# Optimization experiments

Measured on AMD Instinct MI355X. Metric: run time of the kernel, lower is better.

## Reference

```python
import jax, jax.numpy as jnp
import numpy as np

N_NEURONS, D_MODEL, D_FF, N_PATTERNS, K_PATTERNS = 2048, 1024, 4096, 64, 4
B, S, K = 4, 2048, 8


def setup_inputs() -> dict:
    key = jax.random.key(0)
    ks = jax.random.split(key, 10)
    return {
        "x": jax.random.normal(ks[0], (B, S, D_MODEL), jnp.float32),
        "router_out": jax.random.normal(ks[1], (B, S, D_MODEL), jnp.float32),
        "topk_neuron_idx": jax.random.randint(ks[2], (B, S, K), 0, N_NEURONS),
        "topk_neuron_weights": jax.random.uniform(ks[3], (B, S, K), jnp.float32),
        "selected_neurons": jax.random.normal(ks[4], (B, S, K, D_MODEL), jnp.float32),
        "pattern_queries": jax.random.normal(ks[5], (N_PATTERNS, D_MODEL), jnp.float32) * 0.02,
        "gates": jax.random.normal(ks[6], (N_PATTERNS, D_FF), jnp.float32) * 0.02,
        "up_w": jax.random.normal(ks[7], (D_FF, D_MODEL), jnp.float32) / np.sqrt(D_MODEL),
        "up_b": jnp.zeros((D_FF,), jnp.float32),
        "down_w": jax.random.normal(ks[8], (D_MODEL, D_FF), jnp.float32) / np.sqrt(D_FF),
        "down_b": jnp.zeros((D_MODEL,), jnp.float32),
    }


def reference(x, router_out, topk_neuron_idx, topk_neuron_weights, selected_neurons,
              pattern_queries, gates, up_w, up_b, down_w, down_b):
    D = selected_neurons.shape[-1]
    # pattern scoring: [P, B, S, K]
    sim = jnp.einsum('pd,bskd->pbsk', pattern_queries, selected_neurons) / jnp.sqrt(jnp.float32(D))
    pattern_scores = jnp.einsum('pbsk,bsk->bsp', sim, topk_neuron_weights)  # weighted sum over K, permuted
    topk_scores, topk_pattern_idx = jax.lax.top_k(pattern_scores, K_PATTERNS)  # [B,S,k]
    topk_pattern_weights = jax.nn.softmax(topk_scores, axis=-1)
    selected_gates = gates[topk_pattern_idx]  # [B,S,k,d_ff]
    ffn_gate = jnp.einsum('bsk,bskf->bsf', topk_pattern_weights, selected_gates)
    h = jnp.einsum('bsd,fd->bsf', x, up_w) + up_b
    h = jax.nn.gelu(h * jax.nn.sigmoid(ffn_gate), approximate=False)
    return jnp.einsum('bsf,df->bsd', h, down_w) + down_b
```

## Files before the change

### kernel.cpp

```cpp
#include <hip/hip_runtime.h>
#include <hip/hip_bf16.h>
#include <math.h>

#define R_   8192
#define DM   1024
#define DFF  4096
#define NP   64
#define KN   8

typedef __bf16 bf16x8 __attribute__((ext_vector_type(8)));
typedef float  f32x4  __attribute__((ext_vector_type(4)));

__device__ __forceinline__ unsigned short f2bf(float f) {
  union { float f; unsigned u; } v; v.f = f;
  unsigned u = v.u;
  return (unsigned short)((u + 0x7FFFu + ((u >> 16) & 1u)) >> 16);
}

__device__ __forceinline__ float dot4(const float4 a, const float4 b) {
  return a.x * b.x + a.y * b.y + a.z * b.z + a.w * b.w;
}

__device__ __forceinline__ void fma4(float4& a, float w, const float4 s) {
  a.x += w * s.x; a.y += w * s.y; a.z += w * s.z; a.w += w * s.w;
}

__global__ __launch_bounds__(256) void cvt_bf16_kernel(
    const float* __restrict__ in, unsigned short* __restrict__ out, int n8) {
  int i = blockIdx.x * 256 + threadIdx.x;
  if (i >= n8) return;
  const float4* p = (const float4*)in + (size_t)i * 2;
  float4 a = p[0], b = p[1];
  uint4 r;
  r.x = (unsigned)f2bf(a.x) | ((unsigned)f2bf(a.y) << 16);
  r.y = (unsigned)f2bf(a.z) | ((unsigned)f2bf(a.w) << 16);
  r.z = (unsigned)f2bf(b.x) | ((unsigned)f2bf(b.y) << 16);
  r.w = (unsigned)f2bf(b.z) | ((unsigned)f2bf(b.w) << 16);
  ((uint4*)out)[i] = r;
}

__global__ __launch_bounds__(256) void vcomp_kernel(
    const float* __restrict__ sn,
    const float* __restrict__ tw,
    float* __restrict__ v)
{
  const int r = blockIdx.x;
  const int t = threadIdx.x;
  float w[KN];
#pragma unroll
  for (int k = 0; k < KN; ++k) w[k] = tw[(size_t)r * KN + k];
  const float* base = sn + (size_t)r * (KN * DM) + t * 4;
  float4 a = {0.f, 0.f, 0.f, 0.f};
#pragma unroll
  for (int k = 0; k < KN; ++k) fma4(a, w[k], *(const float4*)(base + k * DM));
  *(float4*)(v + (size_t)r * DM + t * 4) = a;
}

__global__ __launch_bounds__(256, 2) void score_kernel(
    const float* __restrict__ v,
    const float* __restrict__ pq,
    int*   __restrict__ out_idx,
    float* __restrict__ out_w)
{
  const int lane = threadIdx.x & 63;
  const int wave = threadIdx.x >> 6;
  const int pos0 = (blockIdx.x * 4 + wave) * 4;

  float4 vr[4][4];
#pragma unroll
  for (int p = 0; p < 4; ++p) {
    const float4* s = (const float4*)(v + (size_t)(pos0 + p) * DM + lane * 16);
    vr[p][0] = s[0]; vr[p][1] = s[1]; vr[p][2] = s[2]; vr[p][3] = s[3];
  }

  float sreg[4];
#pragma unroll 1
  for (int pat = 0; pat < NP; ++pat) {
    const float4* q = (const float4*)(pq + pat * DM + lane * 16);
    const float4 q0 = q[0], q1 = q[1], q2 = q[2], q3 = q[3];
    float part[4];
#pragma unroll
    for (int p = 0; p < 4; ++p)
      part[p] = dot4(q0, vr[p][0]) + dot4(q1, vr[p][1]) +
                dot4(q2, vr[p][2]) + dot4(q3, vr[p][3]);
#pragma unroll
    for (int off = 32; off >= 1; off >>= 1) {
#pragma unroll
      for (int p = 0; p < 4; ++p)
        part[p] += __shfl_xor(part[p], off, 64);
    }
    if (lane == pat) {
#pragma unroll
      for (int p = 0; p < 4; ++p) sreg[p] = part[p] * 0.03125f;
    }
  }

#pragma unroll
  for (int p = 0; p < 4; ++p) {
    float cur = sreg[p];
    float m0, m1, m2, m3; int i0, i1, i2, i3;
#define ARGMAX_STEP(MV, MI)                                   \
    {                                                         \
      float bv = cur; int bi = lane;                          \
      _Pragma("unroll")                                       \
      for (int off = 32; off >= 1; off >>= 1) {               \
        float ov = __shfl_xor(bv, off, 64);                   \
        int   oi = __shfl_xor(bi, off, 64);                   \
        if (ov > bv || (ov == bv && oi < bi)) { bv = ov; bi = oi; } \
      }                                                       \
      MV = bv; MI = bi;                                       \
      if (lane == bi) cur = -3.0e38f;                         \
    }
    ARGMAX_STEP(m0, i0) ARGMAX_STEP(m1, i1) ARGMAX_STEP(m2, i2) ARGMAX_STEP(m3, i3)
#undef ARGMAX_STEP
    const float e1 = __expf(m1 - m0), e2 = __expf(m2 - m0), e3 = __expf(m3 - m0);
    const float inv = 1.f / (1.f + e1 + e2 + e3);
    if (lane < 4) {
      const int r = pos0 + p;
      const int myi = (lane == 0) ? i0 : (lane == 1) ? i1 : (lane == 2) ? i2 : i3;
      const float mye = (lane == 0) ? 1.f : (lane == 1) ? e1 : (lane == 2) ? e2 : e3;
      out_idx[r * 4 + lane] = myi;
      out_w[r * 4 + lane] = mye * inv;
    }
  }
}

__device__ __forceinline__ void gll16(const void* g, void* l) {
  __builtin_amdgcn_global_load_lds(
      (const __attribute__((address_space(1))) unsigned int*)g,
      (__attribute__((address_space(3))) unsigned int*)l, 16, 0, 0);
}

template <int K, int N, int MODE>
__global__ __launch_bounds__(256, 2) void gemm_kernel(
    const unsigned short* __restrict__ A,
    const unsigned short* __restrict__ Bm,
    const float* __restrict__ bias,
    const int*   __restrict__ pidx,
    const float* __restrict__ pwt,
    const float* __restrict__ gates,
    void* __restrict__ Cout)
{
  __shared__ __align__(16) unsigned short As[128 * 32];
  __shared__ __align__(16) unsigned short Bs[128 * 32];
  const int tid  = threadIdx.x;
  const int lane = tid & 63;
  const int wid  = tid >> 6;
  const int wr   = wid >> 1;
  const int wc   = wid & 1;
  constexpr int NB = N / 128;
  const int brow = blockIdx.x / NB;
  const int bcol = blockIdx.x % NB;

  const unsigned short* Ab = A  + (size_t)brow * 128 * K;
  const unsigned short* Bb = Bm + (size_t)bcol * 128 * K;

  f32x4 acc[4][4];
#pragma unroll
  for (int m = 0; m < 4; ++m)
#pragma unroll
    for (int n = 0; n < 4; ++n)
      acc[m][n] = (f32x4){0.f, 0.f, 0.f, 0.f};

  const int srow = tid >> 2;
  const int scol = (tid & 3) * 8;
  char* ldsA = (char*)As + (tid >> 6) * 1024;
  char* ldsB = (char*)Bs + (tid >> 6) * 1024;

  const int arow = wr * 64 + (lane & 15);
  const int bro  = wc * 64 + (lane & 15);
  const int koff = (lane >> 4) * 8;

  for (int k0 = 0; k0 < K; k0 += 32) {
    if (k0) __syncthreads();
    gll16(Ab + (size_t)srow * K + k0 + scol,        ldsA);
    gll16(Ab + (size_t)(srow + 64) * K + k0 + scol, ldsA + 4096);
    gll16(Bb + (size_t)srow * K + k0 + scol,        ldsB);
    gll16(Bb + (size_t)(srow + 64) * K + k0 + scol, ldsB + 4096);
    __syncthreads();

    bf16x8 af[4], bfr[4];
#pragma unroll
    for (int m = 0; m < 4; ++m)
      af[m] = *(const bf16x8*)(As + (arow + m * 16) * 32 + koff);
#pragma unroll
    for (int n = 0; n < 4; ++n)
      bfr[n] = *(const bf16x8*)(Bs + (bro + n * 16) * 32 + koff);
#pragma unroll
    for (int m = 0; m < 4; ++m)
#pragma unroll
      for (int n = 0; n < 4; ++n)
        acc[m][n] = __builtin_amdgcn_mfma_f32_16x16x32_bf16(
            af[m], bfr[n], acc[m][n], 0, 0, 0);
  }

  const int crow0 = brow * 128 + wr * 64;
  const int ccol0 = bcol * 128 + wc * 64 + (lane & 15);
  const int rsub  = (lane >> 4) * 4;

  if (MODE == 0) {
    unsigned short* H = (unsigned short*)Cout;
#pragma unroll
    for (int m = 0; m < 4; ++m) {
      const int rbase = crow0 + m * 16 + rsub;
      int   ia[4][4];
      float wa[4][4];
#pragma unroll
      for (int j = 0; j < 4; ++j) {
        const int4   iq = *(const int4*)(pidx + (size_t)(rbase + j) * 4);
        const float4 wq = *(const float4*)(pwt + (size_t)(rbase + j) * 4);
        ia[j][0] = iq.x; ia[j][1] = iq.y; ia[j][2] = iq.z; ia[j][3] = iq.w;
        wa[j][0] = wq.x; wa[j][1] = wq.y; wa[j][2] = wq.z; wa[j][3] = wq.w;
      }
#pragma unroll
      for (int n = 0; n < 4; ++n) {
        const int col = ccol0 + n * 16;
        const float ub = bias[col];
#pragma unroll
        for (int j = 0; j < 4; ++j) {
          float g = wa[j][0] * gates[(size_t)ia[j][0] * DFF + col]
                  + wa[j][1] * gates[(size_t)ia[j][1] * DFF + col]
                  + wa[j][2] * gates[(size_t)ia[j][2] * DFF + col]
                  + wa[j][3] * gates[(size_t)ia[j][3] * DFF + col];
          const float u   = acc[m][n][j] + ub;
          const float val = u * (1.f / (1.f + __expf(-g)));
          const float h   = 0.5f * val * (1.f + erff(val * 0.70710678118654752f));
          H[(size_t)(rbase + j) * N + col] = f2bf(h);
        }
      }
    }
  } else {
    float* O = (float*)Cout;
#pragma unroll
    for (int m = 0; m < 4; ++m) {
      const int rbase = crow0 + m * 16 + rsub;
#pragma unroll
      for (int n = 0; n < 4; ++n) {
        const int col = ccol0 + n * 16;
        const float db = bias[col];
#pragma unroll
        for (int j = 0; j < 4; ++j)
          O[(size_t)(rbase + j) * N + col] = acc[m][n][j] + db;
      }
    }
  }
}

extern "C" void kernel_launch(void* const* d_in, const int* in_sizes, int n_in,
                              void* d_out, int out_size, void* d_ws, size_t ws_size,
                              hipStream_t stream) {
  const float* x     = (const float*)d_in[0];
  const float* tw    = (const float*)d_in[3];
  const float* sn    = (const float*)d_in[4];
  const float* pq    = (const float*)d_in[5];
  const float* gates = (const float*)d_in[6];
  const float* upw   = (const float*)d_in[7];
  const float* upb   = (const float*)d_in[8];
  const float* dnw   = (const float*)d_in[9];
  const float* dnb   = (const float*)d_in[10];
  float* out = (float*)d_out;

  char* p = (char*)d_ws;
  unsigned short* xb  = (unsigned short*)p; p += (size_t)R_ * DM * 2;
  unsigned short* uwb = (unsigned short*)p; p += (size_t)DFF * DM * 2;
  unsigned short* dwb = (unsigned short*)p; p += (size_t)DM * DFF * 2;
  unsigned short* H   = (unsigned short*)p; p += (size_t)R_ * DFF * 2;
  int*   pidx = (int*)p;   p += (size_t)R_ * 4 * sizeof(int);
  float* pwt  = (float*)p; p += (size_t)R_ * 4 * sizeof(float);
  float* vbuf = (float*)p; p += (size_t)R_ * DM * sizeof(float);

  cvt_bf16_kernel<<<(R_ * DM / 8) / 256, 256, 0, stream>>>(x, xb, R_ * DM / 8);
  cvt_bf16_kernel<<<(DFF * DM / 8) / 256, 256, 0, stream>>>(upw, uwb, DFF * DM / 8);
  cvt_bf16_kernel<<<(DM * DFF / 8) / 256, 256, 0, stream>>>(dnw, dwb, DM * DFF / 8);

  vcomp_kernel<<<R_, 256, 0, stream>>>(sn, tw, vbuf);
  score_kernel<<<R_ / 16, 256, 0, stream>>>(vbuf, pq, pidx, pwt);

  gemm_kernel<DM, DFF, 0><<<(R_ / 128) * (DFF / 128), 256, 0, stream>>>(
      xb, uwb, upb, pidx, pwt, gates, (void*)H);
  gemm_kernel<DFF, DM, 1><<<(R_ / 128) * (DM / 128), 256, 0, stream>>>(
      H, dwb, dnb, nullptr, nullptr, nullptr, (void*)out);
}
```

Measured before the change: 408.5 us.

## Rewrite GEMMs with larger tiles, multi-stage LDS ring and register double-buffering

```diff
diff --git a/kernel.cpp b/kernel.cpp
--- a/kernel.cpp
+++ b/kernel.cpp
@@ -131,8 +131,8 @@
       (__attribute__((address_space(3))) unsigned int*)l, 16, 0, 0);
 }
 
-template <int K, int N, int MODE>
-__global__ __launch_bounds__(256, 2) void gemm_kernel(
+template <int K, int N, int BM, int BN, int WM, int WN, int RING, int MODE>
+__global__ __launch_bounds__(512, 2) void gemm_kernel(
     const unsigned short* __restrict__ A,
     const unsigned short* __restrict__ Bm,
     const float* __restrict__ bias,
@@ -141,67 +141,122 @@
     const float* __restrict__ gates,
     void* __restrict__ Cout)
 {
-  __shared__ __align__(16) unsigned short As[128 * 32];
-  __shared__ __align__(16) unsigned short Bs[128 * 32];
+  extern __shared__ char smem[];
+  constexpr int NT     = K / 32;
+  constexpr int MF     = WM / 16;
+  constexpr int NF     = WN / 16;
+  constexpr int NWC    = BN / WN;
+  constexpr int LA     = BM / 128;
+  constexpr int LB     = BN / 128;
+  constexpr int KEEP   = (RING - 3) * (LA + LB);
+  constexpr int TILE_A = BM * 64;
+  constexpr int TILE   = TILE_A + BN * 64;
+  constexpr int NBN    = N / BN;
+
   const int tid  = threadIdx.x;
   const int lane = tid & 63;
   const int wid  = tid >> 6;
-  const int wr   = wid >> 1;
-  const int wc   = wid & 1;
-  constexpr int NB = N / 128;
-  const int brow = blockIdx.x / NB;
-  const int bcol = blockIdx.x % NB;
-
-  const unsigned short* Ab = A  + (size_t)brow * 128 * K;
-  const unsigned short* Bb = Bm + (size_t)bcol * 128 * K;
-
-  f32x4 acc[4][4];
-#pragma unroll
-  for (int m = 0; m < 4; ++m)
-#pragma unroll
-    for (int n = 0; n < 4; ++n)
+  const int wr   = wid / NWC;
+  const int wc   = wid % NWC;
+
+  const int grid = gridDim.x;
+  const int cpx  = grid >> 3;
+  const int swz  = (blockIdx.x & 7) * cpx + (blockIdx.x >> 3);
+  const int brow = swz / NBN;
+  const int bcol = swz % NBN;
+
+  const unsigned short* Ab = A  + (size_t)brow * BM * K;
+  const unsigned short* Bb = Bm + (size_t)bcol * BN * K;
+
+  int aoffE[LA], boffE[LB];
+#pragma unroll
+  for (int i = 0; i < LA; ++i)
+    aoffE[i] = (i * 128 + wid * 16 + (lane >> 2)) * K + (lane & 3) * 8;
+#pragma unroll
+  for (int i = 0; i < LB; ++i)
+    boffE[i] = (i * 128 + wid * 16 + (lane >> 2)) * K + (lane & 3) * 8;
+
+  const int ard = (wr * WM + (lane & 15)) * 64 + (lane >> 4) * 16;
+  const int brd = (wc * WN + (lane & 15)) * 64 + (lane >> 4) * 16;
+
+  f32x4 acc[MF][NF];
+#pragma unroll
+  for (int m = 0; m < MF; ++m)
+#pragma unroll
+    for (int n = 0; n < NF; ++n)
       acc[m][n] = (f32x4){0.f, 0.f, 0.f, 0.f};
 
-  const int srow = tid >> 2;
-  const int scol = (tid & 3) * 8;
-  char* ldsA = (char*)As + (tid >> 6) * 1024;
-  char* ldsB = (char*)Bs + (tid >> 6) * 1024;
-
-  const int arow = wr * 64 + (lane & 15);
-  const int bro  = wc * 64 + (lane & 15);
-  const int koff = (lane >> 4) * 8;
-
-  for (int k0 = 0; k0 < K; k0 += 32) {
-    if (k0) __syncthreads();
-    gll16(Ab + (size_t)srow * K + k0 + scol,        ldsA);
-    gll16(Ab + (size_t)(srow + 64) * K + k0 + scol, ldsA + 4096);
-    gll16(Bb + (size_t)srow * K + k0 + scol,        ldsB);
-    gll16(Bb + (size_t)(srow + 64) * K + k0 + scol, ldsB + 4096);
-    __syncthreads();
-
-    bf16x8 af[4], bfr[4];
-#pragma unroll
-    for (int m = 0; m < 4; ++m)
-      af[m] = *(const bf16x8*)(As + (arow + m * 16) * 32 + koff);
-#pragma unroll
-    for (int n = 0; n < 4; ++n)
-      bfr[n] = *(const bf16x8*)(Bs + (bro + n * 16) * 32 + koff);
-#pragma unroll
-    for (int m = 0; m < 4; ++m)
-#pragma unroll
-      for (int n = 0; n < 4; ++n)
-        acc[m][n] = __builtin_amdgcn_mfma_f32_16x16x32_bf16(
-            af[m], bfr[n], acc[m][n], 0, 0, 0);
-  }
-
-  const int crow0 = brow * 128 + wr * 64;
-  const int ccol0 = bcol * 128 + wc * 64 + (lane & 15);
+  bf16x8 fa0[MF], fb0[NF], fa1[MF], fb1[NF];
+
+  for (int t = 0; t < RING - 1; ++t) {
+    const int kE = t * 32;
+    char* sba = smem + t * TILE;
+#pragma unroll
+    for (int i = 0; i < LA; ++i)
+      gll16(Ab + kE + aoffE[i], sba + i * 8192 + wid * 1024);
+#pragma unroll
+    for (int i = 0; i < LB; ++i)
+      gll16(Bb + kE + boffE[i], sba + TILE_A + i * 8192 + wid * 1024);
+  }
+  asm volatile("s_waitcnt vmcnt(%0)" ::"i"(KEEP) : "memory");
+  __builtin_amdgcn_s_barrier();
+  {
+    const char* abase = smem + ard;
+    const char* bbase = smem + TILE_A + brd;
+#pragma unroll
+    for (int m = 0; m < MF; ++m) fa0[m] = *(const bf16x8*)(abase + m * 1024);
+#pragma unroll
+    for (int n = 0; n < NF; ++n) fb0[n] = *(const bf16x8*)(bbase + n * 1024);
+  }
+  int rb = 1, sb = RING - 1;
+
+#define GITER(S, FAC, FBC, FAN, FBN)                                          \
+  {                                                                           \
+    if ((S) + 1 < NT) {                                                       \
+      const char* abase = smem + rb * TILE + ard;                             \
+      const char* bbase = smem + rb * TILE + TILE_A + brd;                    \
+      _Pragma("unroll") for (int m = 0; m < MF; ++m)                          \
+        FAN[m] = *(const bf16x8*)(abase + m * 1024);                          \
+      _Pragma("unroll") for (int n = 0; n < NF; ++n)                          \
+        FBN[n] = *(const bf16x8*)(bbase + n * 1024);                          \
+    }                                                                         \
+    if ((S) + RING - 1 < NT) {                                                \
+      const int kE = ((S) + RING - 1) * 32;                                   \
+      char* sba = smem + sb * TILE;                                           \
+      _Pragma("unroll") for (int i = 0; i < LA; ++i)                          \
+        gll16(Ab + kE + aoffE[i], sba + i * 8192 + wid * 1024);               \
+      _Pragma("unroll") for (int i = 0; i < LB; ++i)                          \
+        gll16(Bb + kE + boffE[i], sba + TILE_A + i * 8192 + wid * 1024);      \
+      asm volatile("s_waitcnt vmcnt(%0)" ::"i"(KEEP) : "memory");             \
+    } else {                                                                  \
+      asm volatile("s_waitcnt vmcnt(0)" ::: "memory");                        \
+    }                                                                         \
+    __builtin_amdgcn_s_barrier();                                             \
+    __builtin_amdgcn_s_setprio(1);                                            \
+    _Pragma("unroll") for (int m = 0; m < MF; ++m)                            \
+      _Pragma("unroll") for (int n = 0; n < NF; ++n)                          \
+        acc[m][n] = __builtin_amdgcn_mfma_f32_16x16x32_bf16(                  \
+            FAC[m], FBC[n], acc[m][n], 0, 0, 0);                              \
+    __builtin_amdgcn_s_setprio(0);                                            \
+    __builtin_amdgcn_s_barrier();                                             \
+    rb = rb + 1 == RING ? 0 : rb + 1;                                         \
+    sb = sb + 1 == RING ? 0 : sb + 1;                                         \
+  }
+
+  for (int s = 0; s < NT; s += 2) {
+    GITER(s, fa0, fb0, fa1, fb1);
+    GITER(s + 1, fa1, fb1, fa0, fb0);
+  }
+#undef GITER
+
+  const int crow0 = brow * BM + wr * WM;
+  const int ccol0 = bcol * BN + wc * WN + (lane & 15);
   const int rsub  = (lane >> 4) * 4;
 
   if (MODE == 0) {
     unsigned short* H = (unsigned short*)Cout;
 #pragma unroll
-    for (int m = 0; m < 4; ++m) {
+    for (int m = 0; m < MF; ++m) {
       const int rbase = crow0 + m * 16 + rsub;
       int   ia[4][4];
       float wa[4][4];
@@ -213,7 +268,7 @@
         wa[j][0] = wq.x; wa[j][1] = wq.y; wa[j][2] = wq.z; wa[j][3] = wq.w;
       }
 #pragma unroll
-      for (int n = 0; n < 4; ++n) {
+      for (int n = 0; n < NF; ++n) {
         const int col = ccol0 + n * 16;
         const float ub = bias[col];
 #pragma unroll
@@ -232,10 +287,10 @@
   } else {
     float* O = (float*)Cout;
 #pragma unroll
-    for (int m = 0; m < 4; ++m) {
+    for (int m = 0; m < MF; ++m) {
       const int rbase = crow0 + m * 16 + rsub;
 #pragma unroll
-      for (int n = 0; n < 4; ++n) {
+      for (int n = 0; n < NF; ++n) {
         const int col = ccol0 + n * 16;
         const float db = bias[col];
 #pragma unroll
@@ -276,8 +331,15 @@
   vcomp_kernel<<<R_, 256, 0, stream>>>(sn, tw, vbuf);
   score_kernel<<<R_ / 16, 256, 0, stream>>>(vbuf, pq, pidx, pwt);
 
-  gemm_kernel<DM, DFF, 0><<<(R_ / 128) * (DFF / 128), 256, 0, stream>>>(
+  auto* k1 = gemm_kernel<DM, DFF, 256, 256, 128, 64, 4, 0>;
+  auto* k2 = gemm_kernel<DFF, DM, 256, 128, 64, 64, 6, 1>;
+  hipFuncSetAttribute((const void*)k1, hipFuncAttributeMaxDynamicSharedMemorySize,
+                      4 * (256 + 256) * 64);
+  hipFuncSetAttribute((const void*)k2, hipFuncAttributeMaxDynamicSharedMemorySize,
+                      6 * (256 + 128) * 64);
+
+  k1<<<(R_ / 256) * (DFF / 256), 512, 4 * (256 + 256) * 64, stream>>>(
       xb, uwb, upb, pidx, pwt, gates, (void*)H);
-  gemm_kernel<DFF, DM, 1><<<(R_ / 128) * (DM / 128), 256, 0, stream>>>(
+  k2<<<(R_ / 256) * (DM / 128), 512, 6 * (256 + 128) * 64, stream>>>(
       H, dwb, dnb, nullptr, nullptr, nullptr, (void*)out);
 }
```

Measured after the change: 377.8 us. 7.5% less time.

## Rewrite both GEMMs with larger tiles, double-buffered LDS, swizzle and phased scheduling

Applied to the files above, without the earlier changes.

```diff
diff --git a/kernel.cpp b/kernel.cpp
--- a/kernel.cpp
+++ b/kernel.cpp
@@ -131,117 +131,214 @@
       (__attribute__((address_space(3))) unsigned int*)l, 16, 0, 0);
 }
 
-template <int K, int N, int MODE>
-__global__ __launch_bounds__(256, 2) void gemm_kernel(
+
+#define RD4(D, P)                                                           \
+  { _Pragma("unroll") for (int i_ = 0; i_ < 4; ++i_)                        \
+      D[i_] = *(const bf16x8*)((P) + i_ * 2048); }
+
+#define STAGEH(GB, LOFF)                                                    \
+  { gll16((GB) + soff0, smem + (LOFF) + wid * 1024);                        \
+    gll16((GB) + soff1, smem + (LOFF) + 8192 + wid * 1024); }
+
+#define PHSYNC(DRAIN)                                                       \
+  __builtin_amdgcn_sched_barrier(0);                                        \
+  if (DRAIN) asm volatile("s_waitcnt vmcnt(0)" ::: "memory");               \
+  __builtin_amdgcn_s_barrier();                                             \
+  asm volatile("s_waitcnt lgkmcnt(0)" ::: "memory");                        \
+  __builtin_amdgcn_sched_barrier(0);                                        \
+  __builtin_amdgcn_s_setprio(1);
+
+#define PHEND                                                               \
+  __builtin_amdgcn_s_setprio(0);                                            \
+  __builtin_amdgcn_s_barrier();                                             \
+  __builtin_amdgcn_sched_barrier(0);
+
+#define MF16(MO, AF, BF)                                                    \
+  _Pragma("unroll") for (int m_ = 0; m_ < 4; ++m_)                          \
+  _Pragma("unroll") for (int n_ = 0; n_ < 4; ++n_)                          \
+    acc[(MO) + m_][n_] = __builtin_amdgcn_mfma_f32_16x16x32_bf16(           \
+        AF[m_], BF[n_], acc[(MO) + m_][n_], 0, 0, 0);
+
+__global__ __launch_bounds__(512, 2) void gemm1_kernel(
     const unsigned short* __restrict__ A,
     const unsigned short* __restrict__ Bm,
     const float* __restrict__ bias,
     const int*   __restrict__ pidx,
     const float* __restrict__ pwt,
     const float* __restrict__ gates,
-    void* __restrict__ Cout)
+    unsigned short* __restrict__ H)
 {
-  __shared__ __align__(16) unsigned short As[128 * 32];
-  __shared__ __align__(16) unsigned short Bs[128 * 32];
-  const int tid  = threadIdx.x;
-  const int lane = tid & 63;
-  const int wid  = tid >> 6;
-  const int wr   = wid >> 1;
-  const int wc   = wid & 1;
-  constexpr int NB = N / 128;
-  const int brow = blockIdx.x / NB;
-  const int bcol = blockIdx.x % NB;
-
-  const unsigned short* Ab = A  + (size_t)brow * 128 * K;
-  const unsigned short* Bb = Bm + (size_t)bcol * 128 * K;
+  extern __shared__ char smem[];
+  constexpr int K_ = 1024, NT = 16;
+  const int tid = threadIdx.x, lane = tid & 63, wid = tid >> 6;
+  const int wr = wid >> 2, wc = wid & 3;
+  const int cpx = gridDim.x >> 3;
+  const int swzb = ((int)blockIdx.x & 7) * cpx + ((int)blockIdx.x >> 3);
+  const int brow = swzb >> 4, bcol = swzb & 15;
+
+  const unsigned short* Ab = A  + (size_t)brow * 256 * K_;
+  const unsigned short* Bb = Bm + (size_t)bcol * 256 * K_;
+
+  const int soff0 = (wid * 8 + (lane >> 3)) * K_ + ((lane & 7) ^ (lane >> 3)) * 8;
+  const int soff1 = soff0 + 64 * K_;
+  const int paoff = wr * 16384 + (lane & 15) * 128;
+  const int pboff = 32768 + (wc >> 1) * 16384 + (wc & 1) * 8192 + (lane & 15) * 128;
+  const int sw0 = ((lane >> 4) ^ (lane & 7)) * 16;
+  const int sw1 = ((4 + (lane >> 4)) ^ (lane & 7)) * 16;
+
+  f32x4 acc[8][4];
+#pragma unroll
+  for (int m = 0; m < 8; ++m)
+#pragma unroll
+    for (int n = 0; n < 4; ++n) acc[m][n] = (f32x4){0.f, 0.f, 0.f, 0.f};
+
+  STAGEH(Ab,            0)
+  STAGEH(Ab + 128 * K_, 16384)
+  STAGEH(Bb,            32768)
+  STAGEH(Bb + 128 * K_, 49152)
+  asm volatile("s_waitcnt vmcnt(0)" ::: "memory");
+  __builtin_amdgcn_s_barrier();
+
+#define KT1_BODY(BB, SB, GUARD, KT)                                         \
+  {                                                                         \
+    const char* pa = smem + (BB) + paoff;                                   \
+    const char* pb = smem + (BB) + pboff;                                   \
+    const unsigned short* At = Ab + ((KT) + 1) * 64;                        \
+    const unsigned short* Bt = Bb + ((KT) + 1) * 64;                        \
+    bf16x8 af[4], bks[4];                                                   \
+                               \
+    RD4(af, pa + sw0) RD4(bks, pb + sw0)                                    \
+    if (GUARD) { STAGEH(At, (SB) + 0) STAGEH(At + 128 * K_, (SB) + 16384) } \
+    PHSYNC(0) MF16(0, af, bks) PHEND                                        \
+                                         \
+    RD4(af, pa + 8192 + sw0)                                                \
+    if (GUARD) { STAGEH(Bt, (SB) + 32768) }                                 \
+    PHSYNC(0) MF16(4, af, bks) PHEND                                        \
+                                  \
+    RD4(af, pa + sw1) RD4(bks, pb + sw1)                                    \
+    if (GUARD) { STAGEH(Bt + 128 * K_, (SB) + 49152) }                      \
+    PHSYNC(0) MF16(0, af, bks) PHEND                                        \
+                                                 \
+    RD4(af, pa + 8192 + sw1)                                                \
+    PHSYNC(1) MF16(4, af, bks) PHEND                                        \
+  }
+
+#pragma unroll 1
+  for (int k2 = 0; k2 < NT / 2; ++k2) {
+    const int kt0 = k2 * 2;
+    KT1_BODY(0,     65536, true,             kt0)
+    KT1_BODY(65536, 0,     (k2 < NT/2 - 1),  kt0 + 1)
+  }
+#undef KT1_BODY
+
+  const int crow0 = brow * 256 + wr * 128;
+  const int ccol0 = bcol * 256 + wc * 64 + (lane & 15);
+  const int rsub  = (lane >> 4) * 4;
+#pragma unroll
+  for (int m = 0; m < 8; ++m) {
+    const int rbase = crow0 + m * 16 + rsub;
+    int   ia[4][4];
+    float wa[4][4];
+#pragma unroll
+    for (int j = 0; j < 4; ++j) {
+      const int4   iq = *(const int4*)(pidx + (size_t)(rbase + j) * 4);
+      const float4 wq = *(const float4*)(pwt + (size_t)(rbase + j) * 4);
+      ia[j][0] = iq.x; ia[j][1] = iq.y; ia[j][2] = iq.z; ia[j][3] = iq.w;
+      wa[j][0] = wq.x; wa[j][1] = wq.y; wa[j][2] = wq.z; wa[j][3] = wq.w;
+    }
+#pragma unroll
+    for (int n = 0; n < 4; ++n) {
+      const int col = ccol0 + n * 16;
+      const float ub = bias[col];
+#pragma unroll
+      for (int j = 0; j < 4; ++j) {
+        float g = wa[j][0] * gates[(size_t)ia[j][0] * DFF + col]
+                + wa[j][1] * gates[(size_t)ia[j][1] * DFF + col]
+                + wa[j][2] * gates[(size_t)ia[j][2] * DFF + col]
+                + wa[j][3] * gates[(size_t)ia[j][3] * DFF + col];
+        const float u   = acc[m][n][j] + ub;
+        const float val = u * (1.f / (1.f + __expf(-g)));
+        const float h   = 0.5f * val * (1.f + erff(val * 0.70710678118654752f));
+        H[(size_t)(rbase + j) * DFF + col] = f2bf(h);
+      }
+    }
+  }
+}
+
+__global__ __launch_bounds__(512, 2) void gemm2_kernel(
+    const unsigned short* __restrict__ A,
+    const unsigned short* __restrict__ Bm,
+    const float* __restrict__ bias,
+    float* __restrict__ O)
+{
+  extern __shared__ char smem[];
+  constexpr int K_ = 4096, NT = 64;
+  const int tid = threadIdx.x, lane = tid & 63, wid = tid >> 6;
+  const int wr = wid >> 1, wc = wid & 1;
+  const int cpx = gridDim.x >> 3;
+  const int swzb = ((int)blockIdx.x & 7) * cpx + ((int)blockIdx.x >> 3);
+  const int brow = swzb >> 3, bcol = swzb & 7;
+
+  const unsigned short* Ab = A  + (size_t)brow * 256 * K_;
+  const unsigned short* Bb = Bm + (size_t)bcol * 128 * K_;
+
+  const int soff0 = (wid * 8 + (lane >> 3)) * K_ + ((lane & 7) ^ (lane >> 3)) * 8;
+  const int soff1 = soff0 + 64 * K_;
+  const int paoff = (wr >> 1) * 16384 + (wr & 1) * 8192 + (lane & 15) * 128;
+  const int pboff = 32768 + wc * 8192 + (lane & 15) * 128;
+  const int sw0 = ((lane >> 4) ^ (lane & 7)) * 16;
+  const int sw1 = ((4 + (lane >> 4)) ^ (lane & 7)) * 16;
 
   f32x4 acc[4][4];
 #pragma unroll
   for (int m = 0; m < 4; ++m)
 #pragma unroll
-    for (int n = 0; n < 4; ++n)
-      acc[m][n] = (f32x4){0.f, 0.f, 0.f, 0.f};
-
-  const int srow = tid >> 2;
-  const int scol = (tid & 3) * 8;
-  char* ldsA = (char*)As + (tid >> 6) * 1024;
-  char* ldsB = (char*)Bs + (tid >> 6) * 1024;
-
-  const int arow = wr * 64 + (lane & 15);
-  const int bro  = wc * 64 + (lane & 15);
-  const int koff = (lane >> 4) * 8;
-
-  for (int k0 = 0; k0 < K; k0 += 32) {
-    if (k0) __syncthreads();
-    gll16(Ab + (size_t)srow * K + k0 + scol,        ldsA);
-    gll16(Ab + (size_t)(srow + 64) * K + k0 + scol, ldsA + 4096);
-    gll16(Bb + (size_t)srow * K + k0 + scol,        ldsB);
-    gll16(Bb + (size_t)(srow + 64) * K + k0 + scol, ldsB + 4096);
-    __syncthreads();
-
-    bf16x8 af[4], bfr[4];
-#pragma unroll
-    for (int m = 0; m < 4; ++m)
-      af[m] = *(const bf16x8*)(As + (arow + m * 16) * 32 + koff);
-#pragma unroll
-    for (int n = 0; n < 4; ++n)
-      bfr[n] = *(const bf16x8*)(Bs + (bro + n * 16) * 32 + koff);
-#pragma unroll
-    for (int m = 0; m < 4; ++m)
-#pragma unroll
-      for (int n = 0; n < 4; ++n)
-        acc[m][n] = __builtin_amdgcn_mfma_f32_16x16x32_bf16(
-            af[m], bfr[n], acc[m][n], 0, 0, 0);
-  }
-
-  const int crow0 = brow * 128 + wr * 64;
+    for (int n = 0; n < 4; ++n) acc[m][n] = (f32x4){0.f, 0.f, 0.f, 0.f};
+
+  STAGEH(Ab,            0)
+  STAGEH(Ab + 128 * K_, 16384)
+  STAGEH(Bb,            32768)
+  asm volatile("s_waitcnt vmcnt(0)" ::: "memory");
+  __builtin_amdgcn_s_barrier();
+
+#define KT2_BODY(BB, SB, GUARD, KT)                                         \
+  {                                                                         \
+    const char* pa = smem + (BB) + paoff;                                   \
+    const char* pb = smem + (BB) + pboff;                                   \
+    const unsigned short* At = Ab + ((KT) + 1) * 64;                        \
+    const unsigned short* Bt = Bb + ((KT) + 1) * 64;                        \
+    bf16x8 af[4], bf[4];                                                    \
+                                \
+    RD4(af, pa + sw0) RD4(bf, pb + sw0)                                     \
+    if (GUARD) { STAGEH(At, (SB) + 0) STAGEH(At + 128 * K_, (SB) + 16384)   \
+                 STAGEH(Bt, (SB) + 32768) }                                 \
+    PHSYNC(0) MF16(0, af, bf) PHEND                                         \
+                                                  \
+    RD4(af, pa + sw1) RD4(bf, pb + sw1)                                     \
+    PHSYNC(1) MF16(0, af, bf) PHEND                                         \
+  }
+
+#pragma unroll 1
+  for (int k2 = 0; k2 < NT / 2; ++k2) {
+    const int kt0 = k2 * 2;
+    KT2_BODY(0,     49152, true,            kt0)
+    KT2_BODY(49152, 0,     (k2 < NT/2 - 1), kt0 + 1)
+  }
+#undef KT2_BODY
+
+  const int crow0 = brow * 256 + wr * 64;
   const int ccol0 = bcol * 128 + wc * 64 + (lane & 15);
   const int rsub  = (lane >> 4) * 4;
-
-  if (MODE == 0) {
-    unsigned short* H = (unsigned short*)Cout;
-#pragma unroll
-    for (int m = 0; m < 4; ++m) {
-      const int rbase = crow0 + m * 16 + rsub;
-      int   ia[4][4];
-      float wa[4][4];
-#pragma unroll
-      for (int j = 0; j < 4; ++j) {
-        const int4   iq = *(const int4*)(pidx + (size_t)(rbase + j) * 4);
-        const float4 wq = *(const float4*)(pwt + (size_t)(rbase + j) * 4);
-        ia[j][0] = iq.x; ia[j][1] = iq.y; ia[j][2] = iq.z; ia[j][3] = iq.w;
-        wa[j][0] = wq.x; wa[j][1] = wq.y; wa[j][2] = wq.z; wa[j][3] = wq.w;
-      }
-#pragma unroll
-      for (int n = 0; n < 4; ++n) {
-        const int col = ccol0 + n * 16;
-        const float ub = bias[col];
-#pragma unroll
-        for (int j = 0; j < 4; ++j) {
-          float g = wa[j][0] * gates[(size_t)ia[j][0] * DFF + col]
-                  + wa[j][1] * gates[(size_t)ia[j][1] * DFF + col]
-                  + wa[j][2] * gates[(size_t)ia[j][2] * DFF + col]
-                  + wa[j][3] * gates[(size_t)ia[j][3] * DFF + col];
-          const float u   = acc[m][n][j] + ub;
-          const float val = u * (1.f / (1.f + __expf(-g)));
-          const float h   = 0.5f * val * (1.f + erff(val * 0.70710678118654752f));
-          H[(size_t)(rbase + j) * N + col] = f2bf(h);
-        }
-      }
-    }
-  } else {
-    float* O = (float*)Cout;
-#pragma unroll
-    for (int m = 0; m < 4; ++m) {
-      const int rbase = crow0 + m * 16 + rsub;
-#pragma unroll
-      for (int n = 0; n < 4; ++n) {
-        const int col = ccol0 + n * 16;
-        const float db = bias[col];
-#pragma unroll
-        for (int j = 0; j < 4; ++j)
-          O[(size_t)(rbase + j) * N + col] = acc[m][n][j] + db;
-      }
+#pragma unroll
+  for (int m = 0; m < 4; ++m) {
+    const int rbase = crow0 + m * 16 + rsub;
+#pragma unroll
+    for (int n = 0; n < 4; ++n) {
+      const int col = ccol0 + n * 16;
+      const float db = bias[col];
+#pragma unroll
+      for (int j = 0; j < 4; ++j)
+        O[(size_t)(rbase + j) * DM + col] = acc[m][n][j] + db;
     }
   }
 }
@@ -276,8 +373,13 @@
   vcomp_kernel<<<R_, 256, 0, stream>>>(sn, tw, vbuf);
   score_kernel<<<R_ / 16, 256, 0, stream>>>(vbuf, pq, pidx, pwt);
 
-  gemm_kernel<DM, DFF, 0><<<(R_ / 128) * (DFF / 128), 256, 0, stream>>>(
-      xb, uwb, upb, pidx, pwt, gates, (void*)H);
-  gemm_kernel<DFF, DM, 1><<<(R_ / 128) * (DM / 128), 256, 0, stream>>>(
-      H, dwb, dnb, nullptr, nullptr, nullptr, (void*)out);
-}
+  hipFuncSetAttribute((const void*)gemm1_kernel,
+                      hipFuncAttributeMaxDynamicSharedMemorySize, 131072);
+  hipFuncSetAttribute((const void*)gemm2_kernel,
+                      hipFuncAttributeMaxDynamicSharedMemorySize, 98304);
+
+  gemm1_kernel<<<(R_ / 256) * (DFF / 256), 512, 131072, stream>>>(
+      xb, uwb, upb, pidx, pwt, gates, H);
+  gemm2_kernel<<<(R_ / 256) * (DM / 128), 512, 98304, stream>>>(
+      H, dwb, dnb, out);
+}
```

New measurement: 409.4 us. No clear change (+0.2%).

## Pipeline both GEMMs with multi-stage LDS buffers, swizzled layout and block remap

Applied to the files above, without the earlier changes.

```diff
diff --git a/kernel.cpp b/kernel.cpp
--- a/kernel.cpp
+++ b/kernel.cpp
@@ -131,117 +131,215 @@
       (__attribute__((address_space(3))) unsigned int*)l, 16, 0, 0);
 }
 
-template <int K, int N, int MODE>
-__global__ __launch_bounds__(256, 2) void gemm_kernel(
+
+#define LGKM0 asm volatile("s_waitcnt lgkmcnt(0)" ::: "memory")
+#define VMC(N) asm volatile("s_waitcnt vmcnt(%0)" ::"i"(N) : "memory")
+
+__global__ __launch_bounds__(256, 2) void gemm1_kernel(
     const unsigned short* __restrict__ A,
     const unsigned short* __restrict__ Bm,
     const float* __restrict__ bias,
     const int*   __restrict__ pidx,
     const float* __restrict__ pwt,
     const float* __restrict__ gates,
-    void* __restrict__ Cout)
+    unsigned short* __restrict__ H)
 {
-  __shared__ __align__(16) unsigned short As[128 * 32];
-  __shared__ __align__(16) unsigned short Bs[128 * 32];
-  const int tid  = threadIdx.x;
-  const int lane = tid & 63;
-  const int wid  = tid >> 6;
-  const int wr   = wid >> 1;
-  const int wc   = wid & 1;
-  constexpr int NB = N / 128;
-  const int brow = blockIdx.x / NB;
-  const int bcol = blockIdx.x % NB;
-
-  const unsigned short* Ab = A  + (size_t)brow * 128 * K;
-  const unsigned short* Bb = Bm + (size_t)bcol * 128 * K;
+  extern __shared__ char smem[];
+  constexpr int K_ = 1024, NT = 32;
+  const int tid = threadIdx.x, lane = tid & 63, wid = tid >> 6;
+  const int wr = wid >> 1, wc = wid & 1;
+  const int cpx = gridDim.x >> 3;
+  const int swzb = ((int)blockIdx.x & 7) * cpx + ((int)blockIdx.x >> 3);
+  const int brow = swzb >> 5, bcol = swzb & 31;
+
+  const unsigned short* Ab = A  + (size_t)brow * 256 * K_;
+  const unsigned short* Bb = Bm + (size_t)bcol * 128 * K_;
+
+  const int aSrc = (wid * 16 + (lane >> 2)) * K_ +
+                   (((lane & 3) ^ ((lane >> 2) & 3)) * 8);
+  const int ldsSt = wid * 1024;
+  const int laneRd = (lane & 15) * 64 + (((lane >> 4) ^ (lane & 3)) * 16);
+  const int aRd = wr * 8192 + laneRd;
+  const int bRd = 16384 + wc * 4096 + laneRd;
+
+  f32x4 acc[8][4];
+#pragma unroll
+  for (int m = 0; m < 8; ++m)
+#pragma unroll
+    for (int n = 0; n < 4; ++n) acc[m][n] = (f32x4){0.f, 0.f, 0.f, 0.f};
+
+#define G1_STA(BO, PG) { _Pragma("unroll") for (int i_ = 0; i_ < 4; ++i_)     \
+    gll16((PG) + i_ * 64 * K_ + aSrc, smem + (BO) + i_ * 4096 + ldsSt); }
+#define G1_STB(BO, PG) { _Pragma("unroll") for (int i_ = 0; i_ < 2; ++i_)     \
+    gll16((PG) + i_ * 64 * K_ + aSrc, smem + (BO) + 16384 + i_ * 4096 + ldsSt); }
+
+  G1_STA(0, Ab)           G1_STB(0, Bb)
+  G1_STA(24576, Ab + 32)  G1_STB(24576, Bb + 32)
+  G1_STB(49152, Bb + 64)
+  VMC(8);
+  __builtin_amdgcn_s_barrier();
+
+  int o0 = 0, o1 = 24576, o2 = 49152;
+#pragma unroll 1
+  for (int j = 0; j < NT; ++j) {
+    bf16x8 a[4], b[4];
+    {
+      const char* pa = smem + o0 + aRd;
+      const char* pb = smem + o0 + bRd;
+#pragma unroll
+      for (int m = 0; m < 4; ++m) a[m] = *(const bf16x8*)(pa + m * 1024);
+#pragma unroll
+      for (int n = 0; n < 4; ++n) b[n] = *(const bf16x8*)(pb + n * 1024);
+    }
+    if (j < NT - 2) G1_STA(o2, Ab + (j + 2) * 32)
+    LGKM0;
+    __builtin_amdgcn_s_barrier();
+    __builtin_amdgcn_s_setprio(1);
+#pragma unroll
+    for (int m = 0; m < 4; ++m)
+#pragma unroll
+      for (int n = 0; n < 4; ++n)
+        acc[m][n] = __builtin_amdgcn_mfma_f32_16x16x32_bf16(a[m], b[n], acc[m][n], 0, 0, 0);
+    __builtin_amdgcn_s_setprio(0);
+    {
+      const char* pa = smem + o0 + aRd + 4096;
+#pragma unroll
+      for (int m = 0; m < 4; ++m) a[m] = *(const bf16x8*)(pa + m * 1024);
+    }
+    if (j < NT - 3) G1_STB(o0, Bb + (j + 3) * 32)
+    LGKM0;
+    if (j < NT - 2) { VMC(6); } else { VMC(0); }
+    __builtin_amdgcn_s_barrier();
+    __builtin_amdgcn_s_setprio(1);
+#pragma unroll
+    for (int m = 0; m < 4; ++m)
+#pragma unroll
+      for (int n = 0; n < 4; ++n)
+        acc[4 + m][n] = __builtin_amdgcn_mfma_f32_16x16x32_bf16(a[m], b[n], acc[4 + m][n], 0, 0, 0);
+    __builtin_amdgcn_s_setprio(0);
+    const int t = o0; o0 = o1; o1 = o2; o2 = t;
+  }
+#undef G1_STA
+#undef G1_STB
+
+  const int crow0 = brow * 256 + wr * 128;
+  const int ccol0 = bcol * 128 + wc * 64 + (lane & 15);
+  const int rsub  = (lane >> 4) * 4;
+#pragma unroll
+  for (int m = 0; m < 8; ++m) {
+    const int rbase = crow0 + m * 16 + rsub;
+    int   ia[4][4];
+    float wa[4][4];
+#pragma unroll
+    for (int j = 0; j < 4; ++j) {
+      const int4   iq = *(const int4*)(pidx + (size_t)(rbase + j) * 4);
+      const float4 wq = *(const float4*)(pwt + (size_t)(rbase + j) * 4);
+      ia[j][0] = iq.x; ia[j][1] = iq.y; ia[j][2] = iq.z; ia[j][3] = iq.w;
+      wa[j][0] = wq.x; wa[j][1] = wq.y; wa[j][2] = wq.z; wa[j][3] = wq.w;
+    }
+#pragma unroll
+    for (int n = 0; n < 4; ++n) {
+      const int col = ccol0 + n * 16;
+      const float ub = bias[col];
+#pragma unroll
+      for (int j = 0; j < 4; ++j) {
+        float g = wa[j][0] * gates[(size_t)ia[j][0] * DFF + col]
+                + wa[j][1] * gates[(size_t)ia[j][1] * DFF + col]
+                + wa[j][2] * gates[(size_t)ia[j][2] * DFF + col]
+                + wa[j][3] * gates[(size_t)ia[j][3] * DFF + col];
+        const float u   = acc[m][n][j] + ub;
+        const float val = u * (1.f / (1.f + __expf(-g)));
+        const float h   = 0.5f * val * (1.f + erff(val * 0.70710678118654752f));
+        H[(size_t)(rbase + j) * DFF + col] = f2bf(h);
+      }
+    }
+  }
+}
+
+__global__ __launch_bounds__(256, 2) void gemm2_kernel(
+    const unsigned short* __restrict__ A,
+    const unsigned short* __restrict__ Bm,
+    const float* __restrict__ bias,
+    float* __restrict__ O)
+{
+  extern __shared__ char smem[];
+  constexpr int K_ = 4096, NT = 128;
+  const int tid = threadIdx.x, lane = tid & 63, wid = tid >> 6;
+  const int wr = wid >> 1, wc = wid & 1;
+  const int cpx = gridDim.x >> 3;
+  const int swzb = ((int)blockIdx.x & 7) * cpx + ((int)blockIdx.x >> 3);
+  const int brow = swzb >> 3, bcol = swzb & 7;
+
+  const unsigned short* Ab = A  + (size_t)brow * 128 * K_;
+  const unsigned short* Bb = Bm + (size_t)bcol * 128 * K_;
+
+  const int aSrc = (wid * 16 + (lane >> 2)) * K_ +
+                   (((lane & 3) ^ ((lane >> 2) & 3)) * 8);
+  const int ldsSt = wid * 1024;
+  const int laneRd = (lane & 15) * 64 + (((lane >> 4) ^ (lane & 3)) * 16);
+  const int aRd = wr * 4096 + laneRd;
+  const int bRd = 8192 + wc * 4096 + laneRd;
 
   f32x4 acc[4][4];
 #pragma unroll
   for (int m = 0; m < 4; ++m)
 #pragma unroll
-    for (int n = 0; n < 4; ++n)
-      acc[m][n] = (f32x4){0.f, 0.f, 0.f, 0.f};
-
-  const int srow = tid >> 2;
-  const int scol = (tid & 3) * 8;
-  char* ldsA = (char*)As + (tid >> 6) * 1024;
-  char* ldsB = (char*)Bs + (tid >> 6) * 1024;
-
-  const int arow = wr * 64 + (lane & 15);
-  const int bro  = wc * 64 + (lane & 15);
-  const int koff = (lane >> 4) * 8;
-
-  for (int k0 = 0; k0 < K; k0 += 32) {
-    if (k0) __syncthreads();
-    gll16(Ab + (size_t)srow * K + k0 + scol,        ldsA);
-    gll16(Ab + (size_t)(srow + 64) * K + k0 + scol, ldsA + 4096);
-    gll16(Bb + (size_t)srow * K + k0 + scol,        ldsB);
-    gll16(Bb + (size_t)(srow + 64) * K + k0 + scol, ldsB + 4096);
-    __syncthreads();
-
-    bf16x8 af[4], bfr[4];
+    for (int n = 0; n < 4; ++n) acc[m][n] = (f32x4){0.f, 0.f, 0.f, 0.f};
+
+#define G2_ST(BO, PGA, PGB) {                                                 \
+    _Pragma("unroll") for (int i_ = 0; i_ < 2; ++i_)                          \
+      gll16((PGA) + i_ * 64 * K_ + aSrc, smem + (BO) + i_ * 4096 + ldsSt);    \
+    _Pragma("unroll") for (int i_ = 0; i_ < 2; ++i_)                          \
+      gll16((PGB) + i_ * 64 * K_ + aSrc, smem + (BO) + 8192 + i_ * 4096 + ldsSt); }
+
+  G2_ST(0,     Ab,      Bb)
+  G2_ST(16384, Ab + 32, Bb + 32)
+  G2_ST(32768, Ab + 64, Bb + 64)
+  VMC(8);
+  __builtin_amdgcn_s_barrier();
+
+  int o0 = 0, o1 = 16384, o2 = 32768, o3 = 49152;
+#pragma unroll 1
+  for (int j = 0; j < NT; ++j) {
+    bf16x8 a[4], b[4];
+    {
+      const char* pa = smem + o0 + aRd;
+      const char* pb = smem + o0 + bRd;
+#pragma unroll
+      for (int m = 0; m < 4; ++m) a[m] = *(const bf16x8*)(pa + m * 1024);
+#pragma unroll
+      for (int n = 0; n < 4; ++n) b[n] = *(const bf16x8*)(pb + n * 1024);
+    }
+    if (j < NT - 3) G2_ST(o3, Ab + (j + 3) * 32, Bb + (j + 3) * 32)
+    LGKM0;
+    if (j < NT - 3)      { VMC(8); }
+    else if (j == NT - 3){ VMC(4); }
+    else                 { VMC(0); }
+    __builtin_amdgcn_s_barrier();
+    __builtin_amdgcn_s_setprio(1);
 #pragma unroll
     for (int m = 0; m < 4; ++m)
-      af[m] = *(const bf16x8*)(As + (arow + m * 16) * 32 + koff);
-#pragma unroll
-    for (int n = 0; n < 4; ++n)
-      bfr[n] = *(const bf16x8*)(Bs + (bro + n * 16) * 32 + koff);
-#pragma unroll
-    for (int m = 0; m < 4; ++m)
 #pragma unroll
       for (int n = 0; n < 4; ++n)
-        acc[m][n] = __builtin_amdgcn_mfma_f32_16x16x32_bf16(
-            af[m], bfr[n], acc[m][n], 0, 0, 0);
-  }
+        acc[m][n] = __builtin_amdgcn_mfma_f32_16x16x32_bf16(a[m], b[n], acc[m][n], 0, 0, 0);
+    __builtin_amdgcn_s_setprio(0);
+    const int t = o0; o0 = o1; o1 = o2; o2 = o3; o3 = t;
+  }
+#undef G2_ST
 
   const int crow0 = brow * 128 + wr * 64;
   const int ccol0 = bcol * 128 + wc * 64 + (lane & 15);
   const int rsub  = (lane >> 4) * 4;
-
-  if (MODE == 0) {
-    unsigned short* H = (unsigned short*)Cout;
-#pragma unroll
-    for (int m = 0; m < 4; ++m) {
-      const int rbase = crow0 + m * 16 + rsub;
-      int   ia[4][4];
-      float wa[4][4];
-#pragma unroll
-      for (int j = 0; j < 4; ++j) {
-        const int4   iq = *(const int4*)(pidx + (size_t)(rbase + j) * 4);
-        const float4 wq = *(const float4*)(pwt + (size_t)(rbase + j) * 4);
-        ia[j][0] = iq.x; ia[j][1] = iq.y; ia[j][2] = iq.z; ia[j][3] = iq.w;
-        wa[j][0] = wq.x; wa[j][1] = wq.y; wa[j][2] = wq.z; wa[j][3] = wq.w;
-      }
-#pragma unroll
-      for (int n = 0; n < 4; ++n) {
-        const int col = ccol0 + n * 16;
-        const float ub = bias[col];
-#pragma unroll
-        for (int j = 0; j < 4; ++j) {
-          float g = wa[j][0] * gates[(size_t)ia[j][0] * DFF + col]
-                  + wa[j][1] * gates[(size_t)ia[j][1] * DFF + col]
-                  + wa[j][2] * gates[(size_t)ia[j][2] * DFF + col]
-                  + wa[j][3] * gates[(size_t)ia[j][3] * DFF + col];
-          const float u   = acc[m][n][j] + ub;
-          const float val = u * (1.f / (1.f + __expf(-g)));
-          const float h   = 0.5f * val * (1.f + erff(val * 0.70710678118654752f));
-          H[(size_t)(rbase + j) * N + col] = f2bf(h);
-        }
-      }
-    }
-  } else {
-    float* O = (float*)Cout;
-#pragma unroll
-    for (int m = 0; m < 4; ++m) {
-      const int rbase = crow0 + m * 16 + rsub;
-#pragma unroll
-      for (int n = 0; n < 4; ++n) {
-        const int col = ccol0 + n * 16;
-        const float db = bias[col];
-#pragma unroll
-        for (int j = 0; j < 4; ++j)
-          O[(size_t)(rbase + j) * N + col] = acc[m][n][j] + db;
-      }
+#pragma unroll
+  for (int m = 0; m < 4; ++m) {
+    const int rbase = crow0 + m * 16 + rsub;
+#pragma unroll
+    for (int n = 0; n < 4; ++n) {
+      const int col = ccol0 + n * 16;
+      const float db = bias[col];
+#pragma unroll
+      for (int j = 0; j < 4; ++j)
+        O[(size_t)(rbase + j) * DM + col] = acc[m][n][j] + db;
     }
   }
 }
@@ -276,8 +374,13 @@
   vcomp_kernel<<<R_, 256, 0, stream>>>(sn, tw, vbuf);
   score_kernel<<<R_ / 16, 256, 0, stream>>>(vbuf, pq, pidx, pwt);
 
-  gemm_kernel<DM, DFF, 0><<<(R_ / 128) * (DFF / 128), 256, 0, stream>>>(
-      xb, uwb, upb, pidx, pwt, gates, (void*)H);
-  gemm_kernel<DFF, DM, 1><<<(R_ / 128) * (DM / 128), 256, 0, stream>>>(
-      H, dwb, dnb, nullptr, nullptr, nullptr, (void*)out);
-}
+  hipFuncSetAttribute((const void*)gemm1_kernel,
+                      hipFuncAttributeMaxDynamicSharedMemorySize, 73728);
+  hipFuncSetAttribute((const void*)gemm2_kernel,
+                      hipFuncAttributeMaxDynamicSharedMemorySize, 65536);
+
+  gemm1_kernel<<<(R_ / 256) * (DFF / 128), 256, 73728, stream>>>(
+      xb, uwb, upb, pidx, pwt, gates, H);
+  gemm2_kernel<<<(R_ / 128) * (DM / 128), 256, 65536, stream>>>(
+      H, dwb, dnb, out);
+}
```

Result: faster. 369.2 us (-9.6%).
